# Kernel tuning notes

Hardware: AMD Instinct MI355X
Metric: run time of the kernel (lower is better)

## Reference

```python
import jax, jax.numpy as jnp
import numpy as np

N, C, P, NC, F = 1024, 256, 512, 9, 768
Q = P * (NC + 1)  # scalar output multiplicity (structurally zero: no 0e x 1o -> 0e path)


def setup_inputs():
    key = jax.random.key(0)
    ks = jax.random.split(key, 8)
    s = lambda k, shape, fan: jax.random.normal(k, shape, jnp.float32) / np.sqrt(fan)
    return {
        "encoding": jax.random.normal(ks[0], (N, 3 * C), jnp.float32),
        "W0": s(ks[1], (C, F), C), "b0": jnp.zeros((F,), jnp.float32),
        "g0": jnp.ones((F,), jnp.float32), "be0": jnp.zeros((F,), jnp.float32),
        "W1": s(ks[2], (F, F), F), "b1": jnp.zeros((F,), jnp.float32),
        "g1": jnp.ones((F,), jnp.float32), "be1": jnp.zeros((F,), jnp.float32),
        "Wout": s(ks[3], (F, C), F), "bout": jnp.zeros((C,), jnp.float32),
        "Wtp": jax.random.normal(ks[4], (C, C, P), jnp.float32),
        "num_graphs": N,
    }


def _ln(x, g, b):
    mu = jnp.mean(x, axis=-1, keepdims=True)
    var = jnp.var(x, axis=-1, keepdims=True)
    return (x - mu) * jax.lax.rsqrt(var + 1e-5) * g + b


def reference(encoding, W0, b0, g0, be0, W1, b1, g1, be1, Wout, bout, Wtp, num_graphs):
    v = encoding.reshape(num_graphs, C, 3)           # C x 1o vector features
    r = jnp.linalg.norm(v, axis=-1)                  # [N, C] rotation-invariant norms
    # radial MLP (2 hidden layers, LayerNorm + GELU), dropout=0 (eval)
    h = jax.nn.gelu(_ln(r @ W0 + b0, g0, be0))
    h = jax.nn.gelu(_ln(h @ W1 + b1, g1, be1))
    r_dec = h @ Wout + bout                          # [N, C] scalars (C x 0e)
    # FullyConnectedTensorProduct(Cx0e, Cx1o -> Px1o): uvw weights, CG(0,1,1)=I,
    # path normalization 1/sqrt(mul1*mul2) = 1/C
    t = jnp.einsum('bi,ijp->bjp', r_dec, Wtp)        # [N, C, P]
    out_vec = jnp.einsum('bjp,bjm->bpm', t, v) / C   # [N, P, 3]
    out = jnp.concatenate(
        [out_vec.reshape(num_graphs, 3 * P),
         jnp.zeros((num_graphs, Q), out_vec.dtype)], axis=-1)  # P x 1o + Q x 0e layout
    return out
```

## Files before the change

### kernel.cpp

```cpp
#include <hip/hip_runtime.h>
#include <hip/hip_bf16.h>


#define N_G   1024
#define C_DIM 256
#define P_DIM 512
#define F_DIM 768
#define OUT_STRIDE 6656
#define VEC_LEN 1536

typedef short  short8  __attribute__((ext_vector_type(8)));
typedef float  f32x16  __attribute__((ext_vector_type(16)));

#define GLOAD_LDS16(GP, LP)                                                    \
  __builtin_amdgcn_global_load_lds(                                            \
      (const __attribute__((address_space(1))) void*)(GP),                     \
      (__attribute__((address_space(3))) void*)(LP), 16, 0, 0)

static __device__ __forceinline__ unsigned short f32_bf16(float f){
  unsigned u = __builtin_bit_cast(unsigned, f);
  u = (u + 0x7fffu + ((u >> 16) & 1u)) >> 16;
  return (unsigned short)u;
}

static __device__ __forceinline__ float gelu_tanh(float x){
  float u = 0.7978845608028654f * (x + 0.044715f * x * x * x);
  return 0.5f * x * (1.0f + tanhf(u));
}

__global__ __launch_bounds__(256) void k_prepack(const float* __restrict__ wtp,
                                                 unsigned short* __restrict__ frag){
  int tid  = blockIdx.x * 256 + threadIdx.x;
  int unit = tid >> 6, lane = tid & 63;
  int j  = unit >> 8;
  int pt = (unit >> 4) & 15;
  int ik = unit & 15;
  int p  = pt * 32 + (lane & 31);
  int i0 = ik * 16 + (lane >> 5) * 8;
  const float* src = wtp + (size_t)i0 * (C_DIM * P_DIM) + j * P_DIM + p;
  short8 v;
  #pragma unroll
  for (int e = 0; e < 8; ++e)
    v[e] = (short)f32_bf16(src[(size_t)e * (C_DIM * P_DIM)]);
  *reinterpret_cast<short8*>(frag + (size_t)unit * 512 + lane * 8) = v;
}

__global__ __launch_bounds__(256) void k_norm(const float* __restrict__ enc,
                                              float* __restrict__ r){
  int b = blockIdx.x, t = threadIdx.x;
  const float* e = enc + (size_t)b * F_DIM + t * 3;
  r[(size_t)b * C_DIM + t] = sqrtf(e[0]*e[0] + e[1]*e[1] + e[2]*e[2]);
}

template<bool OBF>
__global__ __launch_bounds__(64) void k_gemm(const float* __restrict__ A,
    const float* __restrict__ B, const float* __restrict__ bias,
    float* __restrict__ C, unsigned short* __restrict__ Cb,
    int M, int N, int K){
  __shared__ __align__(16) float Ast[64][20];
  __shared__ __align__(16) float Bs[64][64];
  int nbc = N >> 6;
  int mb = blockIdx.x / nbc, nb = blockIdx.x % nbc;
  int m0 = mb * 16, n0 = nb * 64;
  int t  = threadIdx.x;
  int cg = t & 15, rg = t >> 4;

  float acc[4][4];
  #pragma unroll
  for (int i = 0; i < 4; ++i)
    #pragma unroll
    for (int jj = 0; jj < 4; ++jj) acc[i][jj] = 0.f;

  int nch = K >> 6;
  for (int ch = 0; ch < nch; ++ch){
    int k0 = ch << 6;
    #pragma unroll
    for (int it = 0; it < 16; ++it)
      Ast[t][it] = A[(size_t)(m0 + it) * K + k0 + t];
    #pragma unroll
    for (int it = 0; it < 64; ++it)
      Bs[it][t] = B[(size_t)(k0 + it) * N + n0 + t];
    __syncthreads();
    #pragma unroll 8
    for (int kk = 0; kk < 64; ++kk){
      float4 av = *reinterpret_cast<const float4*>(&Ast[kk][rg * 4]);
      float4 bv = *reinterpret_cast<const float4*>(&Bs[kk][cg * 4]);
      acc[0][0] += av.x*bv.x; acc[0][1] += av.x*bv.y; acc[0][2] += av.x*bv.z; acc[0][3] += av.x*bv.w;
      acc[1][0] += av.y*bv.x; acc[1][1] += av.y*bv.y; acc[1][2] += av.y*bv.z; acc[1][3] += av.y*bv.w;
      acc[2][0] += av.z*bv.x; acc[2][1] += av.z*bv.y; acc[2][2] += av.z*bv.z; acc[2][3] += av.z*bv.w;
      acc[3][0] += av.w*bv.x; acc[3][1] += av.w*bv.y; acc[3][2] += av.w*bv.z; acc[3][3] += av.w*bv.w;
    }
    __syncthreads();
  }

  #pragma unroll
  for (int i = 0; i < 4; ++i){
    int row = m0 + rg * 4 + i;
    #pragma unroll
    for (int jj = 0; jj < 4; ++jj){
      int col = n0 + cg * 4 + jj;
      float val = acc[i][jj] + bias[col];
      if (OBF) Cb[(size_t)row * N + col] = f32_bf16(val);
      else     C [(size_t)row * N + col] = val;
    }
  }
}

__global__ __launch_bounds__(256) void k_ln(const float* __restrict__ X,
    const float* __restrict__ g, const float* __restrict__ be,
    float* __restrict__ Y){
  int w = threadIdx.x >> 6, lane = threadIdx.x & 63;
  int row = blockIdx.x * 4 + w;
  const float* x = X + (size_t)row * F_DIM;
  float v[12];
  float s = 0.f, s2 = 0.f;
  #pragma unroll
  for (int i = 0; i < 12; ++i){
    v[i] = x[lane + i * 64];
    s += v[i]; s2 += v[i] * v[i];
  }
  #pragma unroll
  for (int off = 32; off; off >>= 1){ s += __shfl_down(s, off); s2 += __shfl_down(s2, off); }
  s = __shfl(s, 0); s2 = __shfl(s2, 0);
  float mu = s * (1.0f / F_DIM);
  float rs = rsqrtf(s2 * (1.0f / F_DIM) - mu * mu + 1e-5f);
  float* y = Y + (size_t)row * F_DIM;
  #pragma unroll
  for (int i = 0; i < 12; ++i){
    int c = lane + i * 64;
    y[c] = gelu_tanh((v[i] - mu) * rs * g[c] + be[c]);
  }
}

__global__ __launch_bounds__(512, 2) void k_tp(const unsigned short* __restrict__ frag,
    const unsigned short* __restrict__ rdec, const float* __restrict__ enc,
    float* __restrict__ part){
  __shared__ unsigned short As[2][8192];
  int bx   = blockIdx.x;
  int pt   = bx & 15;
  int bblk = (bx >> 4) & 3;
  int js   = bx >> 6;
  int w    = threadIdx.x >> 6;
  int lane = threadIdx.x & 63;
  int b    = bblk * 256 + w * 32 + (lane & 31);
  int g    = lane >> 5;

  short8 bf[16];
  #pragma unroll
  for (int ik = 0; ik < 16; ++ik)
    bf[ik] = *reinterpret_cast<const short8*>(rdec + (size_t)b * C_DIM + ik * 16 + g * 8);

  float oacc[48];
  #pragma unroll
  for (int q = 0; q < 48; ++q) oacc[q] = 0.f;

  int j0 = js * 64;
  #define STAGE(BUF, J) do {                                                        \
    _Pragma("unroll")                                                               \
    for (int uu = 0; uu < 2; ++uu){                                                 \
      int u = w * 2 + uu;                                                           \
      const unsigned short* gp = frag + ((size_t)(((J) * 16 + pt) * 16 + u)) * 512  \
                                 + lane * 8;                                        \
      GLOAD_LDS16(gp, &As[BUF][u * 512]);                                           \
    } } while (0)

  STAGE(0, j0);
  __syncthreads();
  int cur = 0;
  for (int j = j0; j < j0 + 64; ++j){
    if (j < j0 + 63) STAGE(cur ^ 1, j + 1);
    f32x16 acc = {};
    #pragma unroll
    for (int ik = 0; ik < 16; ++ik){
      short8 a = *reinterpret_cast<const short8*>(&As[cur][ik * 512 + lane * 8]);
      acc = __builtin_amdgcn_mfma_f32_32x32x16_bf16(a, bf[ik], acc, 0, 0, 0);
    }
    const float* vp = enc + (size_t)b * F_DIM + j * 3;
    float v0 = vp[0], v1 = vp[1], v2 = vp[2];
    #pragma unroll
    for (int r = 0; r < 16; ++r){
      oacc[r*3+0] += acc[r] * v0;
      oacc[r*3+1] += acc[r] * v1;
      oacc[r*3+2] += acc[r] * v2;
    }
    __syncthreads();
    cur ^= 1;
  }

  float* pb = part + (size_t)(js * N_G + b) * VEC_LEN;
  #pragma unroll
  for (int r = 0; r < 16; ++r){
    int p = pt * 32 + (r & 3) + 8 * (r >> 2) + 4 * g;
    pb[p*3+0] = oacc[r*3+0];
    pb[p*3+1] = oacc[r*3+1];
    pb[p*3+2] = oacc[r*3+2];
  }
}

__global__ __launch_bounds__(256) void k_reduce(const float* __restrict__ part,
                                                float* __restrict__ out){
  int idx = blockIdx.x * 256 + threadIdx.x;
  if (idx >= N_G * OUT_STRIDE) return;
  int b = idx / OUT_STRIDE;
  int q = idx - b * OUT_STRIDE;
  float val = 0.f;
  if (q < VEC_LEN){
    size_t base = (size_t)b * VEC_LEN + q;
    const size_t st = (size_t)N_G * VEC_LEN;
    val = (part[base] + part[base + st] + part[base + 2*st] + part[base + 3*st]) * (1.0f / C_DIM);
  }
  out[idx] = val;
}

extern "C" void kernel_launch(void* const* d_in, const int* in_sizes, int n_in,
                              void* d_out, int out_size, void* d_ws, size_t ws_size,
                              hipStream_t stream){
  const float* enc  = (const float*)d_in[0];
  const float* W0   = (const float*)d_in[1];
  const float* b0   = (const float*)d_in[2];
  const float* g0   = (const float*)d_in[3];
  const float* be0  = (const float*)d_in[4];
  const float* W1   = (const float*)d_in[5];
  const float* b1   = (const float*)d_in[6];
  const float* g1   = (const float*)d_in[7];
  const float* be1  = (const float*)d_in[8];
  const float* Wout = (const float*)d_in[9];
  const float* bout = (const float*)d_in[10];
  const float* Wtp  = (const float*)d_in[11];
  float* out = (float*)d_out;

  char* ws = (char*)d_ws;
  unsigned short* frag = (unsigned short*)(ws);
  unsigned short* rdec = (unsigned short*)(ws + 67108864);
  float*          part = (float*)(ws + 67633152);
  float* rbuf = (float*)(ws + 67633152);
  float* bufA = (float*)(ws + 67633152 + 1048576);
  float* bufB = (float*)(ws + 67633152 + 1048576 + 3145728);

  hipLaunchKernelGGL(k_prepack, dim3(16384), dim3(256), 0, stream, Wtp, frag);
  hipLaunchKernelGGL(k_norm,    dim3(N_G),   dim3(256), 0, stream, enc, rbuf);
  hipLaunchKernelGGL((k_gemm<false>), dim3(64 * 12), dim3(64), 0, stream,
                     rbuf, W0, b0, bufA, rdec, N_G, F_DIM, C_DIM);
  hipLaunchKernelGGL(k_ln,      dim3(256),   dim3(256), 0, stream, bufA, g0, be0, bufB);
  hipLaunchKernelGGL((k_gemm<false>), dim3(64 * 12), dim3(64), 0, stream,
                     bufB, W1, b1, bufA, rdec, N_G, F_DIM, F_DIM);
  hipLaunchKernelGGL(k_ln,      dim3(256),   dim3(256), 0, stream, bufA, g1, be1, bufB);
  hipLaunchKernelGGL((k_gemm<true>),  dim3(64 * 4),  dim3(64), 0, stream,
                     bufB, Wout, bout, bufA, rdec, N_G, C_DIM, F_DIM);
  hipLaunchKernelGGL(k_tp,      dim3(256),   dim3(512), 0, stream, frag, rdec, enc, part);
  hipLaunchKernelGGL(k_reduce,  dim3((N_G * OUT_STRIDE + 255) / 256), dim3(256), 0, stream,
                     part, out);
}
```

Before: 433.0 us.

## Restructure tensor-product kernel with K-split waves, transposed vectors, bf16 partials, wider GEMM blocks

```diff
diff --git a/kernel.cpp b/kernel.cpp
--- a/kernel.cpp
+++ b/kernel.cpp
@@ -22,7 +22,9 @@
   u = (u + 0x7fffu + ((u >> 16) & 1u)) >> 16;
   return (unsigned short)u;
 }
-
+static __device__ __forceinline__ float bf16_f32(unsigned short u){
+  return __builtin_bit_cast(float, (unsigned)u << 16);
+}
 static __device__ __forceinline__ float gelu_tanh(float x){
   float u = 0.7978845608028654f * (x + 0.044715f * x * x * x);
   return 0.5f * x * (1.0f + tanhf(u));
@@ -52,54 +54,70 @@
   r[(size_t)b * C_DIM + t] = sqrtf(e[0]*e[0] + e[1]*e[1] + e[2]*e[2]);
 }
 
+__global__ __launch_bounds__(256) void k_vt(const float* __restrict__ enc,
+                                            float* __restrict__ vT){
+  int tid = blockIdx.x * 256 + threadIdx.x;
+  int b  = tid & 1023;
+  int jm = tid >> 10;
+  int j  = jm / 3, m = jm - j * 3;
+  vT[(size_t)j * 3072 + m * 1024 + b] = enc[(size_t)b * F_DIM + j * 3 + m];
+}
+
 template<bool OBF>
-__global__ __launch_bounds__(64) void k_gemm(const float* __restrict__ A,
+__global__ __launch_bounds__(256) void k_gemm(const float* __restrict__ A,
     const float* __restrict__ B, const float* __restrict__ bias,
     float* __restrict__ C, unsigned short* __restrict__ Cb,
     int M, int N, int K){
-  __shared__ __align__(16) float Ast[64][20];
+  __shared__ __align__(16) float Ast[64][36];
   __shared__ __align__(16) float Bs[64][64];
   int nbc = N >> 6;
   int mb = blockIdx.x / nbc, nb = blockIdx.x % nbc;
-  int m0 = mb * 16, n0 = nb * 64;
+  int m0 = mb * 32, n0 = nb * 64;
   int t  = threadIdx.x;
-  int cg = t & 15, rg = t >> 4;
-
-  float acc[4][4];
-  #pragma unroll
-  for (int i = 0; i < 4; ++i)
-    #pragma unroll
-    for (int jj = 0; jj < 4; ++jj) acc[i][jj] = 0.f;
-
-  int nch = K >> 6;
-  for (int ch = 0; ch < nch; ++ch){
-    int k0 = ch << 6;
-    #pragma unroll
-    for (int it = 0; it < 16; ++it)
-      Ast[t][it] = A[(size_t)(m0 + it) * K + k0 + t];
-    #pragma unroll
-    for (int it = 0; it < 64; ++it)
-      Bs[it][t] = B[(size_t)(k0 + it) * N + n0 + t];
-    __syncthreads();
-    #pragma unroll 8
+  int tr = t >> 4, tc = t & 15;
+
+  float acc[2][4];
+  #pragma unroll
+  for (int i = 0; i < 2; ++i)
+    #pragma unroll
+    for (int q = 0; q < 4; ++q) acc[i][q] = 0.f;
+
+  for (int kc = 0; kc < K; kc += 64){
+    {
+      int m = t >> 3, k0 = (t & 7) * 8;
+      const float* ap = A + (size_t)(m0 + m) * K + kc + k0;
+      float4 a0 = *reinterpret_cast<const float4*>(ap);
+      float4 a1 = *reinterpret_cast<const float4*>(ap + 4);
+      Ast[k0+0][m] = a0.x; Ast[k0+1][m] = a0.y; Ast[k0+2][m] = a0.z; Ast[k0+3][m] = a0.w;
+      Ast[k0+4][m] = a1.x; Ast[k0+5][m] = a1.y; Ast[k0+6][m] = a1.z; Ast[k0+7][m] = a1.w;
+    }
+    {
+      int kk = t >> 2, nc = (t & 3) * 16;
+      const float* bp = B + (size_t)(kc + kk) * N + n0 + nc;
+      float4* d = reinterpret_cast<float4*>(&Bs[kk][nc]);
+      d[0] = reinterpret_cast<const float4*>(bp)[0];
+      d[1] = reinterpret_cast<const float4*>(bp)[1];
+      d[2] = reinterpret_cast<const float4*>(bp)[2];
+      d[3] = reinterpret_cast<const float4*>(bp)[3];
+    }
+    __syncthreads();
+    #pragma unroll 16
     for (int kk = 0; kk < 64; ++kk){
-      float4 av = *reinterpret_cast<const float4*>(&Ast[kk][rg * 4]);
-      float4 bv = *reinterpret_cast<const float4*>(&Bs[kk][cg * 4]);
+      float2 av = *reinterpret_cast<const float2*>(&Ast[kk][tr * 2]);
+      float4 bv = *reinterpret_cast<const float4*>(&Bs[kk][tc * 4]);
       acc[0][0] += av.x*bv.x; acc[0][1] += av.x*bv.y; acc[0][2] += av.x*bv.z; acc[0][3] += av.x*bv.w;
       acc[1][0] += av.y*bv.x; acc[1][1] += av.y*bv.y; acc[1][2] += av.y*bv.z; acc[1][3] += av.y*bv.w;
-      acc[2][0] += av.z*bv.x; acc[2][1] += av.z*bv.y; acc[2][2] += av.z*bv.z; acc[2][3] += av.z*bv.w;
-      acc[3][0] += av.w*bv.x; acc[3][1] += av.w*bv.y; acc[3][2] += av.w*bv.z; acc[3][3] += av.w*bv.w;
-    }
-    __syncthreads();
-  }
-
-  #pragma unroll
-  for (int i = 0; i < 4; ++i){
-    int row = m0 + rg * 4 + i;
-    #pragma unroll
-    for (int jj = 0; jj < 4; ++jj){
-      int col = n0 + cg * 4 + jj;
-      float val = acc[i][jj] + bias[col];
+    }
+    __syncthreads();
+  }
+
+  #pragma unroll
+  for (int i = 0; i < 2; ++i){
+    int row = m0 + tr * 2 + i;
+    #pragma unroll
+    for (int q = 0; q < 4; ++q){
+      int col = n0 + tc * 4 + q;
+      float val = acc[i][q] + bias[col];
       if (OBF) Cb[(size_t)row * N + col] = f32_bf16(val);
       else     C [(size_t)row * N + col] = val;
     }
@@ -133,71 +151,115 @@
 }
 
 __global__ __launch_bounds__(512, 2) void k_tp(const unsigned short* __restrict__ frag,
-    const unsigned short* __restrict__ rdec, const float* __restrict__ enc,
-    float* __restrict__ part){
-  __shared__ unsigned short As[2][8192];
+    const unsigned short* __restrict__ rdec, const float* __restrict__ vT,
+    unsigned short* __restrict__ part){
+  __shared__ __align__(16) unsigned short As[2][16384];
   int bx   = blockIdx.x;
   int pt   = bx & 15;
   int bblk = (bx >> 4) & 3;
   int js   = bx >> 6;
   int w    = threadIdx.x >> 6;
   int lane = threadIdx.x & 63;
-  int b    = bblk * 256 + w * 32 + (lane & 31);
+  int bg   = w >> 1, kh = w & 1;
   int g    = lane >> 5;
-
-  short8 bf[16];
-  #pragma unroll
-  for (int ik = 0; ik < 16; ++ik)
-    bf[ik] = *reinterpret_cast<const short8*>(rdec + (size_t)b * C_DIM + ik * 16 + g * 8);
-
-  float oacc[48];
-  #pragma unroll
-  for (int q = 0; q < 48; ++q) oacc[q] = 0.f;
+  int b0   = bblk * 256 + bg * 64 + (lane & 31);
+
+  short8 bf[2][8];
+  #pragma unroll
+  for (int bt = 0; bt < 2; ++bt)
+    #pragma unroll
+    for (int k = 0; k < 8; ++k)
+      bf[bt][k] = *reinterpret_cast<const short8*>(
+          rdec + (size_t)(b0 + bt * 32) * C_DIM + (kh * 8 + k) * 16 + g * 8);
+
+  float oacc[2][48];
+  #pragma unroll
+  for (int bt = 0; bt < 2; ++bt)
+    #pragma unroll
+    for (int q = 0; q < 48; ++q) oacc[bt][q] = 0.f;
 
   int j0 = js * 64;
-  #define STAGE(BUF, J) do {                                                        \
-    _Pragma("unroll")                                                               \
-    for (int uu = 0; uu < 2; ++uu){                                                 \
-      int u = w * 2 + uu;                                                           \
-      const unsigned short* gp = frag + ((size_t)(((J) * 16 + pt) * 16 + u)) * 512  \
-                                 + lane * 8;                                        \
-      GLOAD_LDS16(gp, &As[BUF][u * 512]);                                           \
+  #define STAGE2(BUF, J) do {                                                      \
+    _Pragma("unroll")                                                              \
+    for (int uu = 0; uu < 4; ++uu){                                                \
+      int u = w * 4 + uu;                                                          \
+      const unsigned short* gp = frag +                                            \
+          ((size_t)((((J) + (u >> 4)) * 16 + pt) * 16 + (u & 15))) * 512 + lane*8; \
+      GLOAD_LDS16(gp, &As[BUF][u * 512]);                                          \
     } } while (0)
 
-  STAGE(0, j0);
+  STAGE2(0, j0);
   __syncthreads();
   int cur = 0;
-  for (int j = j0; j < j0 + 64; ++j){
-    if (j < j0 + 63) STAGE(cur ^ 1, j + 1);
-    f32x16 acc = {};
-    #pragma unroll
-    for (int ik = 0; ik < 16; ++ik){
-      short8 a = *reinterpret_cast<const short8*>(&As[cur][ik * 512 + lane * 8]);
-      acc = __builtin_amdgcn_mfma_f32_32x32x16_bf16(a, bf[ik], acc, 0, 0, 0);
-    }
-    const float* vp = enc + (size_t)b * F_DIM + j * 3;
-    float v0 = vp[0], v1 = vp[1], v2 = vp[2];
-    #pragma unroll
-    for (int r = 0; r < 16; ++r){
-      oacc[r*3+0] += acc[r] * v0;
-      oacc[r*3+1] += acc[r] * v1;
-      oacc[r*3+2] += acc[r] * v2;
+  for (int jj = j0; jj < j0 + 64; jj += 2){
+    if (jj + 2 < j0 + 64) STAGE2(cur ^ 1, jj + 2);
+    #pragma unroll
+    for (int jl = 0; jl < 2; ++jl){
+      const unsigned short* ab = &As[cur][(jl * 16 + kh * 8) * 512 + lane * 8];
+      short8 af[8];
+      #pragma unroll
+      for (int k = 0; k < 8; ++k)
+        af[k] = *reinterpret_cast<const short8*>(ab + k * 512);
+      f32x16 acc0 = {}, acc1 = {};
+      #pragma unroll
+      for (int k = 0; k < 8; ++k){
+        acc0 = __builtin_amdgcn_mfma_f32_32x32x16_bf16(af[k], bf[0][k], acc0, 0, 0, 0);
+        acc1 = __builtin_amdgcn_mfma_f32_32x32x16_bf16(af[k], bf[1][k], acc1, 0, 0, 0);
+      }
+      const float* vp = vT + (size_t)(jj + jl) * 3072;
+      float v00 = vp[b0], v01 = vp[1024 + b0], v02 = vp[2048 + b0];
+      float v10 = vp[b0 + 32], v11 = vp[1024 + b0 + 32], v12 = vp[2048 + b0 + 32];
+      #pragma unroll
+      for (int r = 0; r < 16; ++r){
+        oacc[0][r*3+0] += acc0[r]*v00; oacc[0][r*3+1] += acc0[r]*v01; oacc[0][r*3+2] += acc0[r]*v02;
+        oacc[1][r*3+0] += acc1[r]*v10; oacc[1][r*3+1] += acc1[r]*v11; oacc[1][r*3+2] += acc1[r]*v12;
+      }
     }
     __syncthreads();
     cur ^= 1;
   }
 
-  float* pb = part + (size_t)(js * N_G + b) * VEC_LEN;
-  #pragma unroll
-  for (int r = 0; r < 16; ++r){
-    int p = pt * 32 + (r & 3) + 8 * (r >> 2) + 4 * g;
-    pb[p*3+0] = oacc[r*3+0];
-    pb[p*3+1] = oacc[r*3+1];
-    pb[p*3+2] = oacc[r*3+2];
-  }
-}
-
-__global__ __launch_bounds__(256) void k_reduce(const float* __restrict__ part,
+  float* red = (float*)As;
+  int rb = bg >> 1;
+  #pragma unroll
+  for (int round = 0; round < 2; ++round){
+    __syncthreads();
+    if (kh == 1 && rb == round){
+      int chunk = (bg & 1) * 2;
+      #pragma unroll
+      for (int bt = 0; bt < 2; ++bt){
+        float* dst = red + ((size_t)((chunk + bt) * 64 + lane)) * 48;
+        #pragma unroll
+        for (int q = 0; q < 48; ++q) dst[q] = oacc[bt][q];
+      }
+    }
+    __syncthreads();
+    if (kh == 0 && rb == round){
+      int chunk = (bg & 1) * 2;
+      #pragma unroll
+      for (int bt = 0; bt < 2; ++bt){
+        const float* src = red + ((size_t)((chunk + bt) * 64 + lane)) * 48;
+        #pragma unroll
+        for (int q = 0; q < 48; ++q) oacc[bt][q] += src[q];
+      }
+    }
+  }
+  if (kh == 0){
+    #pragma unroll
+    for (int bt = 0; bt < 2; ++bt){
+      unsigned short* pb = part + ((size_t)js * N_G + (b0 + bt * 32)) * VEC_LEN;
+      #pragma unroll
+      for (int r = 0; r < 16; ++r){
+        int p = pt * 32 + (r & 3) + 8 * (r >> 2) + 4 * g;
+        pb[p*3+0] = f32_bf16(oacc[bt][r*3+0]);
+        pb[p*3+1] = f32_bf16(oacc[bt][r*3+1]);
+        pb[p*3+2] = f32_bf16(oacc[bt][r*3+2]);
+      }
+    }
+  }
+}
+
+__global__ __launch_bounds__(256) void k_reduce(const unsigned short* __restrict__ part,
                                                 float* __restrict__ out){
   int idx = blockIdx.x * 256 + threadIdx.x;
   if (idx >= N_G * OUT_STRIDE) return;
@@ -207,7 +269,8 @@
   if (q < VEC_LEN){
     size_t base = (size_t)b * VEC_LEN + q;
     const size_t st = (size_t)N_G * VEC_LEN;
-    val = (part[base] + part[base + st] + part[base + 2*st] + part[base + 3*st]) * (1.0f / C_DIM);
+    val = (bf16_f32(part[base]) + bf16_f32(part[base + st]) +
+           bf16_f32(part[base + 2*st]) + bf16_f32(part[base + 3*st])) * (1.0f / C_DIM);
   }
   out[idx] = val;
 }
@@ -232,22 +295,24 @@
   char* ws = (char*)d_ws;
   unsigned short* frag = (unsigned short*)(ws);
   unsigned short* rdec = (unsigned short*)(ws + 67108864);
-  float*          part = (float*)(ws + 67633152);
-  float* rbuf = (float*)(ws + 67633152);
-  float* bufA = (float*)(ws + 67633152 + 1048576);
-  float* bufB = (float*)(ws + 67633152 + 1048576 + 3145728);
+  float*          vT   = (float*)(ws + 67633152);
+  unsigned short* part = (unsigned short*)(ws + 70778880);
+  float* rbuf = (float*)(ws + 70778880);
+  float* bufA = (float*)(ws + 70778880 + 1048576);
+  float* bufB = (float*)(ws + 70778880 + 1048576 + 3145728);
 
   hipLaunchKernelGGL(k_prepack, dim3(16384), dim3(256), 0, stream, Wtp, frag);
   hipLaunchKernelGGL(k_norm,    dim3(N_G),   dim3(256), 0, stream, enc, rbuf);
-  hipLaunchKernelGGL((k_gemm<false>), dim3(64 * 12), dim3(64), 0, stream,
+  hipLaunchKernelGGL(k_vt,      dim3(3072),  dim3(256), 0, stream, enc, vT);
+  hipLaunchKernelGGL((k_gemm<false>), dim3(32 * 12), dim3(256), 0, stream,
                      rbuf, W0, b0, bufA, rdec, N_G, F_DIM, C_DIM);
   hipLaunchKernelGGL(k_ln,      dim3(256),   dim3(256), 0, stream, bufA, g0, be0, bufB);
-  hipLaunchKernelGGL((k_gemm<false>), dim3(64 * 12), dim3(64), 0, stream,
+  hipLaunchKernelGGL((k_gemm<false>), dim3(32 * 12), dim3(256), 0, stream,
                      bufB, W1, b1, bufA, rdec, N_G, F_DIM, F_DIM);
   hipLaunchKernelGGL(k_ln,      dim3(256),   dim3(256), 0, stream, bufA, g1, be1, bufB);
-  hipLaunchKernelGGL((k_gemm<true>),  dim3(64 * 4),  dim3(64), 0, stream,
+  hipLaunchKernelGGL((k_gemm<true>),  dim3(32 * 4),  dim3(256), 0, stream,
                      bufB, Wout, bout, bufA, rdec, N_G, C_DIM, F_DIM);
-  hipLaunchKernelGGL(k_tp,      dim3(256),   dim3(512), 0, stream, frag, rdec, enc, part);
+  hipLaunchKernelGGL(k_tp,      dim3(256),   dim3(512), 0, stream, frag, rdec, vT, part);
   hipLaunchKernelGGL(k_reduce,  dim3((N_G * OUT_STRIDE + 255) / 256), dim3(256), 0, stream,
                      part, out);
 }
```

Measured after the change: 479.5 us. 1.11x slower.
